# Kernel optimization log

Measured on AMD Instinct MI355X. Metric: run time of the kernel, lower is better.

Reference implementation:

```python
import jax, jax.numpy as jnp
import numpy as np

K = 3  # kernel_size
P = 1  # padding (must satisfy K == 2*P+1 for the original einsum to be shape-valid)


def setup_inputs() -> dict:
    key = jax.random.key(0)
    k1, k2, k3 = jax.random.split(key, 3)
    b, i, c, L, o = 16, 64, 4, 4096, 64
    x = jax.random.normal(k1, (b, i, c, L), dtype=jnp.float32)
    time_tensor = jax.random.uniform(k2, (b, c, L), dtype=jnp.float32)
    weights = jax.random.normal(k3, (o, i, c, K), dtype=jnp.float32)
    return {"x": x, "time_tensor": time_tensor, "weights": weights}


def reference(x, time_tensor, weights):
    """x: (b,i,c,L), time_tensor: (b,c,L), weights: (o,i,c,K) -> (b,o,c,L).

    Faithful to the torch module: pad x/time by P on the time axis, unfold x
    into sliding windows, pad the unfolded tensor again by P, multiply by the
    time scalar per (b,c,l) and contract over (i,k), then crop P from each end.
    The time factor is scalar per output element, so we factor it out of the
    einsum instead of materializing the (b,o,i,c,k,l) dynamic_weights tensor --
    mathematically identical, massively cheaper.
    """
    xp = jnp.pad(x, ((0, 0), (0, 0), (0, 0), (P, P)))            # (b,i,c,L+2P)
    tp = jnp.pad(time_tensor, ((0, 0), (0, 0), (P, P)))          # (b,c,L+2P)
    Lw = xp.shape[-1] - K + 1                                    # == L since K=2P+1
    # unfold -> (b,i,c,K,Lw), matching torch's permute(0,2,1,4,3) after transpose
    xu = jnp.stack([xp[..., j:j + Lw] for j in range(K)], axis=-2)
    xu = jnp.transpose(xu, (0, 2, 1, 3, 4))                      # (b,c,i,K,Lw)
    xu = jnp.pad(xu, ((0, 0), (0, 0), (0, 0), (0, 0), (P, P)))   # (b,c,i,K,Lw+2P)
    conv = jnp.einsum('oick,bcikl->bocl', weights, xu)           # (b,o,c,L+2P)
    out = conv * tp[:, None, :, :]
    return out[..., P:-P]                                        # (b,o,c,L)
```

## Files before the change

### kernel.cpp

```cpp
#include <hip/hip_runtime.h>


#define NB 16
#define NI 64
#define NC 4
#define NL 4096
#define NO 64
#define KW 3
#define LT 64
#define ROWS (LT + 2)
#define ROWB 128

#define W_PACK_BYTES (NO * NI * NC * KW * 2)

typedef float f32x4 __attribute__((ext_vector_type(4)));
typedef short bf16x8 __attribute__((ext_vector_type(8)));
typedef unsigned int u32x2 __attribute__((ext_vector_type(2)));

__device__ inline unsigned short f2bf(float f) {
    unsigned int u = __builtin_bit_cast(unsigned int, f);
    u += 0x7FFFu + ((u >> 16) & 1u);
    return (unsigned short)(u >> 16);
}

__global__ __launch_bounds__(256)
void prepack_w_kernel(const float* __restrict__ w, unsigned short* __restrict__ wp) {
    const int idx  = blockIdx.x * 256 + threadIdx.x;
    const int j    = idx & 7;
    const int lane = (idx >> 3) & 63;
    const int r9   = idx >> 9;
    const int cc   = r9 % 6;
    const int wv   = (r9 / 6) & 3;
    const int c    = r9 / 24;
    const int orow = wv * 16 + (lane & 15);
    const int i    = (cc & 1) * 32 + ((lane >> 4) << 3) + j;
    const int k    = cc >> 1;
    wp[idx] = f2bf(w[((orow * NI + i) * NC + c) * KW + k]);
}

__global__ __launch_bounds__(256)
void tconv_mfma_kernel(const float* __restrict__ x,
                       const float* __restrict__ tt,
                       const unsigned short* __restrict__ wp,
                       float* __restrict__ out)
{
    __shared__ char lds[ROWS * ROWB];

    const int t    = threadIdx.x;
    const int lb   = blockIdx.x * LT;
    const int c    = blockIdx.y;
    const int b    = blockIdx.z;
    const int lane = t & 63;
    const int wave = t >> 6;
    const int o0   = wave * 16;

    bf16x8 wfrag[6];
    {
        const bf16x8* wpb = (const bf16x8*)wp + (size_t)((c * 4 + wave) * 6) * 64 + lane;
#pragma unroll
        for (int cc = 0; cc < 6; ++cc) wfrag[cc] = wpb[cc * 64];
    }

    const float* xb = x + ((size_t)b * NI * NC + c) * NL;
    {
        const int rr = lane + 1;
        const int l  = lb + lane;
        const int swz = (rr & 7) << 4;
#pragma unroll
        for (int it = 0; it < 4; ++it) {
            const int ib = (it * 4 + wave) * 4;
            const float* xi = xb + (size_t)ib * (NC * NL);
            const float a0 = xi[l];
            const float a1 = xi[(size_t)(NC * NL) + l];
            const float a2 = xi[(size_t)(2 * NC * NL) + l];
            const float a3 = xi[(size_t)(3 * NC * NL) + l];
            u32x2 pk;
            pk[0] = (unsigned int)f2bf(a0) | ((unsigned int)f2bf(a1) << 16);
            pk[1] = (unsigned int)f2bf(a2) | ((unsigned int)f2bf(a3) << 16);
            const int off = rr * ROWB + ((2 * ib) ^ swz);
            *(u32x2*)(lds + off) = pk;
        }
    }
    if (t < 128) {
        const int which = t & 1;
        const int i     = t >> 1;
        const int row   = which ? (LT + 1) : 0;
        const int l     = which ? (lb + LT) : (lb - 1);
        const bool ok   = (l >= 0) && (l < NL);
        const float v   = ok ? xb[(size_t)i * (NC * NL) + l] : 0.f;
        const int off = row * ROWB + ((2 * i) ^ ((row & 7) << 4));
        *(unsigned short*)(lds + off) = f2bf(v);
    }
    __syncthreads();

    f32x4 acc[LT / 16] = {};
    const int lcol  = lane & 15;
    const int ksub2 = (lane >> 4) * 16;

#pragma unroll
    for (int lt = 0; lt < LT / 16; ++lt) {
#pragma unroll
        for (int cc = 0; cc < 6; ++cc) {
            const int k    = cc >> 1;
            const int ih   = cc & 1;
            const int row  = lt * 16 + lcol + k;
            const int colb = ih * 64 + ksub2;
            const int off  = row * ROWB + (colb ^ ((row & 7) << 4));
            const bf16x8 xfrag = *(const bf16x8*)(lds + off);
            acc[lt] = __builtin_amdgcn_mfma_f32_16x16x32_bf16(xfrag, wfrag[cc], acc[lt], 0, 0, 0);
        }
    }

    const float* tb = tt + (size_t)(b * NC + c) * NL;
    const int o  = o0 + lcol;
    float* orow = out + ((size_t)b * NO * NC + (size_t)o * NC + c) * NL;
#pragma unroll
    for (int lt = 0; lt < LT / 16; ++lt) {
        const int l0 = lb + lt * 16 + (lane >> 4) * 4;
        const f32x4 tv = *(const f32x4*)(tb + l0);
        f32x4 res;
#pragma unroll
        for (int r = 0; r < 4; ++r) res[r] = acc[lt][r] * tv[r];
        *(f32x4*)(orow + l0) = res;
    }
}

extern "C" void kernel_launch(void* const* d_in, const int* in_sizes, int n_in,
                              void* d_out, int out_size, void* d_ws, size_t ws_size,
                              hipStream_t stream) {
    const float* x  = (const float*)d_in[0];
    const float* tt = (const float*)d_in[1];
    const float* w  = (const float*)d_in[2];
    float* out = (float*)d_out;
    unsigned short* wpck = (unsigned short*)d_ws;

    dim3 block(256);
    prepack_w_kernel<<<dim3(NO * NI * NC * KW / 256), block, 0, stream>>>(w, wpck);

    dim3 grid(NL / LT, NC, NB);
    tconv_mfma_kernel<<<grid, block, 0, stream>>>(x, tt, wpck, out);
}
```

Before: 40.66 us.

## Process two L-tiles per block with register prefetch into double-buffered LDS

Each block now handles two consecutive 64-wide L tiles. The second tile's x values are loaded into registers while the first tile is computed, then written to a second LDS buffer, so global load latency overlaps MFMA work and the weight fragments are loaded once per two tiles. The weight prepack kernel is rewritten to read the fp32 weights coalesced and scatter the bf16 writes instead. The grid is halved, which reduces parallelism and raises register pressure.

```diff
diff --git a/kernel.cpp b/kernel.cpp
--- a/kernel.cpp
+++ b/kernel.cpp
@@ -8,6 +8,7 @@
 #define NO 64
 #define KW 3
 #define LT 64
+#define NT 2
 #define ROWS (LT + 2)
 #define ROWB 128
 
@@ -25,17 +26,98 @@
 
 __global__ __launch_bounds__(256)
 void prepack_w_kernel(const float* __restrict__ w, unsigned short* __restrict__ wp) {
-    const int idx  = blockIdx.x * 256 + threadIdx.x;
-    const int j    = idx & 7;
-    const int lane = (idx >> 3) & 63;
-    const int r9   = idx >> 9;
-    const int cc   = r9 % 6;
-    const int wv   = (r9 / 6) & 3;
-    const int c    = r9 / 24;
-    const int orow = wv * 16 + (lane & 15);
-    const int i    = (cc & 1) * 32 + ((lane >> 4) << 3) + j;
-    const int k    = cc >> 1;
-    wp[idx] = f2bf(w[((orow * NI + i) * NC + c) * KW + k]);
+    const int idx = blockIdx.x * 256 + threadIdx.x;
+    const float v = w[idx];
+    const int k = idx % 3;
+    int r = idx / 3;
+    const int c = r & 3;  r >>= 2;
+    const int i = r & 63;
+    const int o = r >> 6;
+    const int cc   = k * 2 + (i >> 5);
+    const int lane = (((i >> 3) & 3) << 4) | (o & 15);
+    const int j    = i & 7;
+    const int wv   = o >> 4;
+    wp[(((c * 4 + wv) * 6 + cc) * 64 + lane) * 8 + j] = f2bf(v);
+}
+
+__device__ __forceinline__ void load_x(const float* __restrict__ xb, int lb,
+                                       int t, int lane, int wave,
+                                       float s[16], float& h) {
+    const int l = lb + lane;
+#pragma unroll
+    for (int it = 0; it < 4; ++it) {
+        const int ib = (it * 4 + wave) * 4;
+        const float* xi = xb + (size_t)ib * (NC * NL);
+        s[it * 4 + 0] = xi[l];
+        s[it * 4 + 1] = xi[(size_t)(NC * NL) + l];
+        s[it * 4 + 2] = xi[(size_t)(2 * NC * NL) + l];
+        s[it * 4 + 3] = xi[(size_t)(3 * NC * NL) + l];
+    }
+    h = 0.f;
+    if (t < 128) {
+        const int which = t & 1;
+        const int i     = t >> 1;
+        const int lh    = which ? (lb + LT) : (lb - 1);
+        if (lh >= 0 && lh < NL) h = xb[(size_t)i * (NC * NL) + lh];
+    }
+}
+
+__device__ __forceinline__ void write_lds(char* __restrict__ buf,
+                                          int t, int lane, int wave,
+                                          const float s[16], float h) {
+    const int rr  = lane + 1;
+    const int swz = (rr & 7) << 4;
+#pragma unroll
+    for (int it = 0; it < 4; ++it) {
+        const int ib = (it * 4 + wave) * 4;
+        u32x2 pk;
+        pk[0] = (unsigned int)f2bf(s[it * 4 + 0]) | ((unsigned int)f2bf(s[it * 4 + 1]) << 16);
+        pk[1] = (unsigned int)f2bf(s[it * 4 + 2]) | ((unsigned int)f2bf(s[it * 4 + 3]) << 16);
+        *(u32x2*)(buf + rr * ROWB + ((2 * ib) ^ swz)) = pk;
+    }
+    if (t < 128) {
+        const int which = t & 1;
+        const int i     = t >> 1;
+        const int row   = which ? (LT + 1) : 0;
+        *(unsigned short*)(buf + row * ROWB + ((2 * i) ^ ((row & 7) << 4))) = f2bf(h);
+    }
+}
+
+__device__ __forceinline__ void compute_store(const char* __restrict__ buf,
+                                              const bf16x8 wfrag[6],
+                                              const float* __restrict__ tb,
+                                              float* __restrict__ ob,
+                                              int lb, int lane) {
+    const int lcol  = lane & 15;
+    const int ksub2 = (lane >> 4) * 16;
+
+    f32x4 tv[4];
+#pragma unroll
+    for (int lt = 0; lt < 4; ++lt)
+        tv[lt] = *(const f32x4*)(tb + lb + lt * 16 + (lane >> 4) * 4);
+
+    f32x4 acc[4] = {};
+#pragma unroll
+    for (int lt = 0; lt < 4; ++lt) {
+#pragma unroll
+        for (int cc = 0; cc < 6; ++cc) {
+            const int k    = cc >> 1;
+            const int ih   = cc & 1;
+            const int row  = lt * 16 + lcol + k;
+            const int colb = ih * 64 + ksub2;
+            const int off  = row * ROWB + (colb ^ ((row & 7) << 4));
+            const bf16x8 xf = *(const bf16x8*)(buf + off);
+            acc[lt] = __builtin_amdgcn_mfma_f32_16x16x32_bf16(xf, wfrag[cc], acc[lt], 0, 0, 0);
+        }
+    }
+#pragma unroll
+    for (int lt = 0; lt < 4; ++lt) {
+        const int l0 = lb + lt * 16 + (lane >> 4) * 4;
+        f32x4 r;
+#pragma unroll
+        for (int q = 0; q < 4; ++q) r[q] = acc[lt][q] * tv[lt][q];
+        *(f32x4*)(ob + l0) = r;
+    }
 }
 
 __global__ __launch_bounds__(256)
@@ -44,14 +126,15 @@
                        const unsigned short* __restrict__ wp,
                        float* __restrict__ out)
 {
-    __shared__ char lds[ROWS * ROWB];
+    __shared__ char lds[NT][ROWS * ROWB];
 
     const int t    = threadIdx.x;
-    const int lb   = blockIdx.x * LT;
+    const int lane = t & 63;
+    const int wave = t >> 6;
     const int c    = blockIdx.y;
     const int b    = blockIdx.z;
-    const int lane = t & 63;
-    const int wave = t >> 6;
+    const int lb0  = blockIdx.x * (LT * NT);
+    const int lb1  = lb0 + LT;
     const int o0   = wave * 16;
 
     bf16x8 wfrag[6];
@@ -62,67 +145,22 @@
     }
 
     const float* xb = x + ((size_t)b * NI * NC + c) * NL;
-    {
-        const int rr = lane + 1;
-        const int l  = lb + lane;
-        const int swz = (rr & 7) << 4;
-#pragma unroll
-        for (int it = 0; it < 4; ++it) {
-            const int ib = (it * 4 + wave) * 4;
-            const float* xi = xb + (size_t)ib * (NC * NL);
-            const float a0 = xi[l];
-            const float a1 = xi[(size_t)(NC * NL) + l];
-            const float a2 = xi[(size_t)(2 * NC * NL) + l];
-            const float a3 = xi[(size_t)(3 * NC * NL) + l];
-            u32x2 pk;
-            pk[0] = (unsigned int)f2bf(a0) | ((unsigned int)f2bf(a1) << 16);
-            pk[1] = (unsigned int)f2bf(a2) | ((unsigned int)f2bf(a3) << 16);
-            const int off = rr * ROWB + ((2 * ib) ^ swz);
-            *(u32x2*)(lds + off) = pk;
-        }
-    }
-    if (t < 128) {
-        const int which = t & 1;
-        const int i     = t >> 1;
-        const int row   = which ? (LT + 1) : 0;
-        const int l     = which ? (lb + LT) : (lb - 1);
-        const bool ok   = (l >= 0) && (l < NL);
-        const float v   = ok ? xb[(size_t)i * (NC * NL) + l] : 0.f;
-        const int off = row * ROWB + ((2 * i) ^ ((row & 7) << 4));
-        *(unsigned short*)(lds + off) = f2bf(v);
-    }
+    const float* tb = tt + (size_t)(b * NC + c) * NL;
+    float* ob = out + ((size_t)b * NO * NC + (size_t)(o0 + (lane & 15)) * NC + c) * NL;
+
+    float s0[16], h0;
+    load_x(xb, lb0, t, lane, wave, s0, h0);
+    write_lds(&lds[0][0], t, lane, wave, s0, h0);
     __syncthreads();
 
-    f32x4 acc[LT / 16] = {};
-    const int lcol  = lane & 15;
-    const int ksub2 = (lane >> 4) * 16;
+    float s1[16], h1;
+    load_x(xb, lb1, t, lane, wave, s1, h1);
 
-#pragma unroll
-    for (int lt = 0; lt < LT / 16; ++lt) {
-#pragma unroll
-        for (int cc = 0; cc < 6; ++cc) {
-            const int k    = cc >> 1;
-            const int ih   = cc & 1;
-            const int row  = lt * 16 + lcol + k;
-            const int colb = ih * 64 + ksub2;
-            const int off  = row * ROWB + (colb ^ ((row & 7) << 4));
-            const bf16x8 xfrag = *(const bf16x8*)(lds + off);
-            acc[lt] = __builtin_amdgcn_mfma_f32_16x16x32_bf16(xfrag, wfrag[cc], acc[lt], 0, 0, 0);
-        }
-    }
+    compute_store(&lds[0][0], wfrag, tb, ob, lb0, lane);
 
-    const float* tb = tt + (size_t)(b * NC + c) * NL;
-    const int o  = o0 + lcol;
-    float* orow = out + ((size_t)b * NO * NC + (size_t)o * NC + c) * NL;
-#pragma unroll
-    for (int lt = 0; lt < LT / 16; ++lt) {
-        const int l0 = lb + lt * 16 + (lane >> 4) * 4;
-        const f32x4 tv = *(const f32x4*)(tb + l0);
-        f32x4 res;
-#pragma unroll
-        for (int r = 0; r < 4; ++r) res[r] = acc[lt][r] * tv[r];
-        *(f32x4*)(orow + l0) = res;
-    }
+    write_lds(&lds[1][0], t, lane, wave, s1, h1);
+    __syncthreads();
+    compute_store(&lds[1][0], wfrag, tb, ob, lb1, lane);
 }
 
 extern "C" void kernel_launch(void* const* d_in, const int* in_sizes, int n_in,
@@ -137,6 +175,6 @@
     dim3 block(256);
     prepack_w_kernel<<<dim3(NO * NI * NC * KW / 256), block, 0, stream>>>(w, wpck);
 
-    dim3 grid(NL / LT, NC, NB);
+    dim3 grid(NL / (LT * NT), NC, NB);
     tconv_mfma_kernel<<<grid, block, 0, stream>>>(x, tt, wpck, out);
 }
```

Measured after the change: 37.32 us. 1.09x faster.
